# Optimization experiments

Hardware: AMD Instinct MI355X
Metric: run time of the kernel (lower is better)

## Reference

```python
import jax, jax.numpy as jnp
import numpy as np

B, T, D, H = 2, 1024, 1024, 16
HS = D // H
EPS = 1e-5
SCALE = float(np.sqrt(HS))  # faithful bug: scores / hs**(-0.5) == scores * sqrt(hs)


def setup_inputs() -> dict:
    key = jax.random.key(0)
    ks = jax.random.split(key, 20)
    n = lambda k, shape: jax.random.normal(k, shape, dtype=jnp.float32) * 0.02
    return {
        "src": jax.random.normal(ks[0], (B, T, D), dtype=jnp.float32),
        "att": jax.random.normal(ks[1], (B, T, D), dtype=jnp.float32),
        # causal masked self-attention (no biases on q/k/v)
        "wq_m": n(ks[2], (H, D, HS)), "wk_m": n(ks[3], (H, D, HS)), "wv_m": n(ks[4], (H, D, HS)),
        "proj_m_w": n(ks[5], (D, D)), "proj_m_b": jnp.zeros((D,), jnp.float32),
        # final (cross) attention (biases on q/k/v)
        "wq_f": n(ks[6], (H, D, HS)), "wk_f": n(ks[7], (H, D, HS)), "wv_f": n(ks[8], (H, D, HS)),
        "bq_f": jnp.zeros((H, HS), jnp.float32), "bk_f": jnp.zeros((H, HS), jnp.float32),
        "bv_f": jnp.zeros((H, HS), jnp.float32),
        "proj_f_w": n(ks[9], (D, D)), "proj_f_b": jnp.zeros((D,), jnp.float32),
        # FFN
        "w1": n(ks[10], (D, 4 * D)), "b1": jnp.zeros((4 * D,), jnp.float32),
        "w2": n(ks[11], (4 * D, D)), "b2": jnp.zeros((D,), jnp.float32),
        # shared RMSNorm weight (one instance reused at all three sites)
        "norm_w": jnp.ones((D,), jnp.float32),
    }


def rmsnorm(x, w):
    return x * jax.lax.rsqrt(jnp.mean(x * x, axis=-1, keepdims=True) + EPS) * w


def masked_attn(x, wq, wk, wv):
    q = jnp.einsum('btd,hde->bhte', x, wq)
    k = jnp.einsum('btd,hde->bhte', x, wk)
    v = jnp.einsum('btd,hde->bhte', x, wv)
    scores = jnp.einsum('bhte,bhse->bhts', q, k) * SCALE  # [B,H,T,T]
    causal = jnp.tril(jnp.ones((T, T), dtype=bool))
    scores = jnp.where(causal, scores, -jnp.inf)
    a = jax.nn.softmax(scores, axis=-1)
    o = jnp.einsum('bhts,bhse->bhte', a, v)
    return o.transpose(0, 2, 1, 3).reshape(B, T, D)  # concat heads


def final_attn(x, att, wq, bq, wk, bk, wv, bv):
    q = jnp.einsum('btd,hde->bhte', att, wq) + bq[None, :, None, :]
    k = jnp.einsum('btd,hde->bhte', att, wk) + bk[None, :, None, :]
    v = jnp.einsum('btd,hde->bhte', x, wv) + bv[None, :, None, :]
    scores = jnp.einsum('bhte,bhse->bhts', q, k) * SCALE
    a = jax.nn.softmax(scores, axis=-1)
    o = jnp.einsum('bhts,bhse->bhte', a, v)
    return o.transpose(0, 2, 1, 3).reshape(B, T, D)


def reference(src, att, wq_m, wk_m, wv_m, proj_m_w, proj_m_b,
              wq_f, wk_f, wv_f, bq_f, bk_f, bv_f, proj_f_w, proj_f_b,
              w1, b1, w2, b2, norm_w):
    # masked self-attention block
    m = masked_attn(rmsnorm(src, norm_w), wq_m, wk_m, wv_m)
    m_out = src + (m @ proj_m_w + proj_m_b)
    # cross attention block (q/k from norm(att), v from m_out)
    f = final_attn(m_out, rmsnorm(att, norm_w), wq_f, bq_f, wk_f, bk_f, wv_f, bv_f)
    f_out = m_out + (f @ proj_f_w + proj_f_b)
    # FFN block
    h = rmsnorm(f_out, norm_w)
    h = jax.nn.gelu(h @ w1 + b1, approximate=False) @ w2 + b2
    return f_out + h
```

## Files before the change

kernel.cpp:

```cpp
#include <hip/hip_runtime.h>
#include <math.h>

#define BB 2
#define TT 1024
#define DD 1024
#define HH 16
#define HS 64
#define NROWS (BB*TT)

typedef _Float16 f16;
typedef __attribute__((ext_vector_type(8))) _Float16 half8;
typedef __attribute__((ext_vector_type(4))) _Float16 half4;
typedef __attribute__((ext_vector_type(4))) float f32x4;

constexpr float EPS   = 1e-5f;
constexpr float SCALE = 8.0f;

__device__ __forceinline__ void load_lds16(const f16* g, f16* l) {
    __builtin_amdgcn_global_load_lds(
        (const __attribute__((address_space(1))) unsigned int*)g,
        (__attribute__((address_space(3))) unsigned int*)l, 16, 0, 0);
}

__device__ __forceinline__ int xcd_swizzle(int lin, int total) {
    if ((total & 7) == 0) {
        const int chunk = total >> 3;
        lin = (lin & 7) * chunk + (lin >> 3);
    }
    return lin;
}

__global__ __launch_bounds__(256) void prologue_all(
    const float* __restrict__ wq_m, const float* __restrict__ wk_m,
    const float* __restrict__ wv_m, const float* __restrict__ proj_m_w,
    const float* __restrict__ wq_f, const float* __restrict__ wk_f,
    const float* __restrict__ wv_f, const float* __restrict__ proj_f_w,
    const float* __restrict__ w1,   const float* __restrict__ w2,
    f16* __restrict__ wt,
    const float* __restrict__ bq, const float* __restrict__ bk,
    float* __restrict__ biascat,
    const float* __restrict__ src, const float* __restrict__ att,
    const float* __restrict__ normw,
    f16* __restrict__ xn_s, f16* __restrict__ xn_a)
{
    const int bid = blockIdx.x;
    const int tid = threadIdx.x;
    const size_t M_ = 1024 * 1024;

    __shared__ float tt[64][65];

    if (bid == 4096) {
        for (int j = tid; j < 5120; j += 256)
            biascat[j] = (j < 3072) ? 0.f : ((j < 4096) ? bq[j - 3072] : bk[j - 4096]);
        return;
    }

    if (bid > 4096) {
        const int rrow = bid - 4097;
        const int row  = rrow & (NROWS - 1);
        const float* xr = ((rrow < NROWS) ? src : att) + (size_t)row * DD;
        f16* out = ((rrow < NROWS) ? xn_s : xn_a) + (size_t)row * DD;

        float4 xv = reinterpret_cast<const float4*>(xr)[tid];
        float ss = xv.x*xv.x + xv.y*xv.y + xv.z*xv.z + xv.w*xv.w;
        float* red = &tt[0][0];
        red[tid] = ss; __syncthreads();
        for (int s = 128; s > 0; s >>= 1) {
            if (tid < s) red[tid] += red[tid + s];
            __syncthreads();
        }
        const float inv = rsqrtf(red[0] * (1.0f / DD) + EPS);
        float4 wv = reinterpret_cast<const float4*>(normw)[tid];
        half4 o;
        o.x = (f16)(xv.x * inv * wv.x);
        o.y = (f16)(xv.y * inv * wv.y);
        o.z = (f16)(xv.z * inv * wv.z);
        o.w = (f16)(xv.w * inv * wv.w);
        *reinterpret_cast<half4*>(&out[tid * 4]) = o;
        return;
    }

    const float* W; f16* Wt; int K, N, lognk, t; bool headw;
    if (bid < 768)       { const int m = bid >> 8;
                           W = (m == 0) ? wq_m : (m == 1) ? wk_m : wv_m;
                           Wt = wt + (size_t)m * M_;
                           K = 1024; N = 1024; lognk = 4; headw = true;  t = bid & 255; }
    else if (bid < 1024) { W = proj_m_w; Wt = wt + 6 * M_;
                           K = 1024; N = 1024; lognk = 4; headw = false; t = bid - 768; }
    else if (bid < 1792) { const int m = (bid - 1024) >> 8;
                           W = (m == 0) ? wq_f : (m == 1) ? wk_f : wv_f;
                           Wt = wt + (size_t)(3 + m) * M_;
                           K = 1024; N = 1024; lognk = 4; headw = true;  t = (bid - 1024) & 255; }
    else if (bid < 2048) { W = proj_f_w; Wt = wt + 7 * M_;
                           K = 1024; N = 1024; lognk = 4; headw = false; t = bid - 1792; }
    else if (bid < 3072) { W = w1; Wt = wt + 8 * M_;
                           K = 1024; N = 4096; lognk = 4; headw = false; t = bid - 2048; }
    else                 { W = w2; Wt = wt + 12 * M_;
                           K = 4096; N = 1024; lognk = 6; headw = false; t = bid - 3072; }

    const int k0 = (t & ((1 << lognk) - 1)) * 64;
    const int n0 = (t >> lognk) * 64;

    #pragma unroll
    for (int r = 0; r < 4; ++r) {
        const int idx = tid + r * 256;
        const int kl  = idx >> 4;
        const int nl4 = (idx & 15) * 4;
        const float* gp;
        if (headw) {
            gp = W + ((size_t)(n0 >> 6) * K + (k0 + kl)) * 64 + nl4;
        } else {
            gp = W + (size_t)(k0 + kl) * N + n0 + nl4;
        }
        float4 v = *reinterpret_cast<const float4*>(gp);
        tt[kl][nl4 + 0] = v.x; tt[kl][nl4 + 1] = v.y;
        tt[kl][nl4 + 2] = v.z; tt[kl][nl4 + 3] = v.w;
    }
    __syncthreads();
    #pragma unroll
    for (int r = 0; r < 4; ++r) {
        const int idx = tid + r * 256;
        const int nl  = idx >> 4;
        const int kl4 = (idx & 15) * 4;
        half4 o;
        o.x = (f16)tt[kl4 + 0][nl];
        o.y = (f16)tt[kl4 + 1][nl];
        o.z = (f16)tt[kl4 + 2][nl];
        o.w = (f16)tt[kl4 + 3][nl];
        *reinterpret_cast<half4*>(&Wt[(size_t)(n0 + nl) * K + k0 + kl4]) = o;
    }
}

template<int BM, int EPI, bool HEADOUT, bool SPLITA, bool OHALF, bool PARTIAL>
__global__ __launch_bounds__(256, 2) void gemm_mfma(
    const f16* __restrict__ A1,
    const f16* __restrict__ A2,
    const f16* __restrict__ Bt,
    const float* __restrict__ bias,
    float* __restrict__ outF,
    f16* __restrict__ outH,
    int N, int K, int splitN)
{
    constexpr int BK = 32;
    constexpr int MI = 4;
    constexpr int NI = (BM == 128) ? 4 : 2;
    constexpr int WN = (BM == 128) ? 64 : 32;
    constexpr int ASLOT = BM * 4;
    constexpr int AINST = ASLOT / 256;

    __shared__ f16 ldsA[2][ASLOT * 8];
    __shared__ f16 ldsB[2][512 * 8];

    const int tid  = threadIdx.x;
    const int lane = tid & 63;
    const int wid  = tid >> 6;
    const int gy = gridDim.y;
    const int lin = xcd_swizzle(blockIdx.y * gridDim.x + blockIdx.x,
                                gridDim.x * gy);
    const int m0 = (lin % gy) * BM;
    const int n0 = (lin / gy) * 128;
    const int wm = (BM == 128) ? (wid >> 1) : 0;
    const int wn = (BM == 128) ? (wid & 1) : wid;

    const int Klen  = K / gridDim.z;
    const int kbase = blockIdx.z * Klen;

    const f16* Aptr = (SPLITA && n0 >= splitN) ? A2 : A1;

    f32x4 acc[MI][NI];
    #pragma unroll
    for (int i = 0; i < MI; ++i)
        #pragma unroll
        for (int j = 0; j < NI; ++j)
            acc[i][j] = (f32x4){0.f, 0.f, 0.f, 0.f};

    auto stage = [&](int buf, int kt) {
        const int k0 = kbase + kt * BK;
        #pragma unroll
        for (int i = 0; i < AINST; ++i) {
            const int s   = (wid * AINST + i) * 64 + lane;
            const int kh  = s / BM;
            const int row = s % BM;
            load_lds16(Aptr + (size_t)(m0 + row) * K + (k0 + kh * 8),
                       &ldsA[buf][s * 8]);
        }
        #pragma unroll
        for (int i = 0; i < 2; ++i) {
            const int s   = (wid * 2 + i) * 64 + lane;
            const int kh  = s >> 7;
            const int col = s & 127;
            load_lds16(Bt + (size_t)(n0 + col) * K + (k0 + kh * 8),
                       &ldsB[buf][s * 8]);
        }
    };

    const int NT = Klen / BK;
    stage(0, 0);
    __syncthreads();
    int cur = 0;
    const int l15 = lane & 15, l4 = lane >> 4;
    for (int kt = 0; kt < NT; ++kt) {
        if (kt + 1 < NT) stage(cur ^ 1, kt + 1);
        half8 af[MI], bfr[NI];
        #pragma unroll
        for (int mi = 0; mi < MI; ++mi)
            af[mi] = *reinterpret_cast<const half8*>(
                &ldsA[cur][(l4 * BM + wm * 64 + mi * 16 + l15) * 8]);
        #pragma unroll
        for (int ni = 0; ni < NI; ++ni)
            bfr[ni] = *reinterpret_cast<const half8*>(
                &ldsB[cur][(l4 * 128 + wn * WN + ni * 16 + l15) * 8]);
        #pragma unroll
        for (int mi = 0; mi < MI; ++mi)
            #pragma unroll
            for (int ni = 0; ni < NI; ++ni)
                acc[mi][ni] = __builtin_amdgcn_mfma_f32_16x16x32_f16(
                    af[mi], bfr[ni], acc[mi][ni], 0, 0, 0);
        __syncthreads();
        cur ^= 1;
    }

    f16* pout = nullptr;
    if (PARTIAL) {
        const size_t MN = (size_t)gridDim.y * BM * N;
        pout = outH + (size_t)blockIdx.z * MN;
    }

    #pragma unroll
    for (int mi = 0; mi < MI; ++mi) {
        #pragma unroll
        for (int ni = 0; ni < NI; ++ni) {
            #pragma unroll
            for (int r = 0; r < 4; ++r) {
                const int row = m0 + wm * 64 + mi * 16 + l4 * 4 + r;
                const int col = n0 + wn * WN + ni * 16 + l15;
                float v = acc[mi][ni][r];
                if (PARTIAL) {
                    pout[(size_t)row * N + col] = (f16)v;
                    continue;
                }
                if (EPI >= 1) v += bias[col];
                if (EPI == 2) v = 0.5f * v * (1.0f + erff(v * 0.70710678118f));
                size_t oidx;
                if (HEADOUT) {
                    const int mat = col >> 10;
                    const int h = (col >> 6) & 15, e = col & 63;
                    const int b = row >> 10, t = row & (TT - 1);
                    oidx = (size_t)mat * ((size_t)NROWS * DD)
                         + ((size_t)((b * HH + h) * TT + t)) * HS + e;
                } else {
                    oidx = (size_t)row * N + col;
                }
                if (OHALF) outH[oidx] = (f16)v;
                else       outF[oidx] = v;
            }
        }
    }
}

template<int MODE>
__global__ __launch_bounds__(256) void reduce_fuse(const f16* __restrict__ part,
                                                   const float* __restrict__ bias,
                                                   const float* __restrict__ residF,
                                                   const f16* __restrict__ residH,
                                                   float* __restrict__ outF,
                                                   f16* __restrict__ outH,
                                                   const float* __restrict__ normw,
                                                   f16* __restrict__ xnout) {
    const size_t MN  = (size_t)NROWS * 1024;
    const int tid = threadIdx.x;
    const size_t idx = ((size_t)blockIdx.x * 256 + tid) * 4;
    float o[4];
    {
        half4 p0 = *reinterpret_cast<const half4*>(part + idx);
        half4 p1 = *reinterpret_cast<const half4*>(part + MN + idx);
        half4 p2 = *reinterpret_cast<const half4*>(part + 2 * MN + idx);
        half4 p3 = *reinterpret_cast<const half4*>(part + 3 * MN + idx);
        float4 bi = *reinterpret_cast<const float4*>(bias + (idx & 1023));
        o[0] = (float)p0.x + (float)p1.x + (float)p2.x + (float)p3.x + bi.x;
        o[1] = (float)p0.y + (float)p1.y + (float)p2.y + (float)p3.y + bi.y;
        o[2] = (float)p0.z + (float)p1.z + (float)p2.z + (float)p3.z + bi.z;
        o[3] = (float)p0.w + (float)p1.w + (float)p2.w + (float)p3.w + bi.w;
    }
    if (MODE == 0 || MODE == 2) {
        float4 rs = *reinterpret_cast<const float4*>(residF + idx);
        o[0] += rs.x; o[1] += rs.y; o[2] += rs.z; o[3] += rs.w;
    } else {
        half4 rh = *reinterpret_cast<const half4*>(residH + idx);
        o[0] += (float)rh.x; o[1] += (float)rh.y; o[2] += (float)rh.z; o[3] += (float)rh.w;
    }

    if (MODE == 0) {
        half4 h;
        h.x = (f16)o[0]; h.y = (f16)o[1]; h.z = (f16)o[2]; h.w = (f16)o[3];
        *reinterpret_cast<half4*>(outH + idx) = h;
        return;
    }

    float4 ov = {o[0], o[1], o[2], o[3]};
    *reinterpret_cast<float4*>(outF + idx) = ov;

    if (MODE == 1) {
        __shared__ float red[256];
        red[tid] = o[0]*o[0] + o[1]*o[1] + o[2]*o[2] + o[3]*o[3];
        __syncthreads();
        for (int s = 128; s > 0; s >>= 1) {
            if (tid < s) red[tid] += red[tid + s];
            __syncthreads();
        }
        const float inv = rsqrtf(red[0] * (1.0f / DD) + EPS);
        float4 nw = *reinterpret_cast<const float4*>(normw + (idx & 1023));
        half4 h;
        h.x = (f16)(o[0] * inv * nw.x);
        h.y = (f16)(o[1] * inv * nw.y);
        h.z = (f16)(o[2] * inv * nw.z);
        h.w = (f16)(o[3] * inv * nw.w);
        *reinterpret_cast<half4*>(xnout + idx) = h;
    }
}

__global__ __launch_bounds__(256) void reduce_gelu(const f16* __restrict__ part,
                                                   const float* __restrict__ b1,
                                                   f16* __restrict__ h1out) {
    const size_t MN  = (size_t)NROWS * 4096;
    const size_t idx = ((size_t)blockIdx.x * 256 + threadIdx.x) * 4;
    half4 p0 = *reinterpret_cast<const half4*>(part + idx);
    half4 p1 = *reinterpret_cast<const half4*>(part + MN + idx);
    float4 bi = *reinterpret_cast<const float4*>(b1 + (idx & 4095));
    float o[4];
    o[0] = (float)p0.x + (float)p1.x + bi.x;
    o[1] = (float)p0.y + (float)p1.y + bi.y;
    o[2] = (float)p0.z + (float)p1.z + bi.z;
    o[3] = (float)p0.w + (float)p1.w + bi.w;
    half4 h;
    #pragma unroll
    for (int j = 0; j < 4; ++j)
        o[j] = 0.5f * o[j] * (1.0f + erff(o[j] * 0.70710678118f));
    h.x = (f16)o[0]; h.y = (f16)o[1]; h.z = (f16)o[2]; h.w = (f16)o[3];
    *reinterpret_cast<half4*>(h1out + idx) = h;
}

template<bool CAUSAL>
__global__ __launch_bounds__(256) void attn_mfma(const f16* __restrict__ Q,
                                                 const f16* __restrict__ Kg,
                                                 const f16* __restrict__ Vg,
                                                 f16* __restrict__ O) {
    const int iq  = blockIdx.x;
    const int bh  = blockIdx.y;
    const int tid = threadIdx.x;
    const int lane = tid & 63;
    const int w   = tid >> 6;
    const int l15 = lane & 15, l4 = lane >> 4;

    __shared__ f16 Ks[512 * 8];
    __shared__ f16 VT[64 * 72];
    __shared__ f16 Ps[4][16 * 72];

    const f16* qb = Q  + ((size_t)bh * TT + (size_t)iq * 64) * HS;
    const f16* kb = Kg + (size_t)bh * TT * HS;
    const f16* vb = Vg + (size_t)bh * TT * HS;

    half8 qf[2];
    #pragma unroll
    for (int ks = 0; ks < 2; ++ks)
        qf[ks] = *reinterpret_cast<const half8*>(
            qb + (size_t)(w * 16 + l15) * HS + ks * 32 + l4 * 8);

    f32x4 oacc[4];
    #pragma unroll
    for (int ni = 0; ni < 4; ++ni) oacc[ni] = (f32x4){0.f, 0.f, 0.f, 0.f};
    float m_run[4], l_run[4];
    #pragma unroll
    for (int r = 0; r < 4; ++r) { m_run[r] = -1e30f; l_run[r] = 0.f; }

    const int sp  = lane & 31;
    const int ehv = lane >> 5;
    const int c0  = w * 16 + ehv * 8;

    const int ntiles = CAUSAL ? (iq + 1) : (TT / 64);
    for (int js = 0; js < ntiles; ++js) {
        __syncthreads();

        #pragma unroll
        for (int i = 0; i < 2; ++i) {
            const int slot = (w * 2 + i) * 64 + lane;
            load_lds16(kb + (size_t)(js * 64 + (slot & 63)) * HS + (slot >> 6) * 8,
                       &Ks[slot * 8]);
        }
        {
            const f16* vrow = vb + (size_t)(js * 64 + 2 * sp) * HS + c0;
            uint4 r0 = *reinterpret_cast<const uint4*>(vrow);
            uint4 r1 = *reinterpret_cast<const uint4*>(vrow + HS);
            const unsigned rc0[4] = {r0.x, r0.y, r0.z, r0.w};
            const unsigned rc1[4] = {r1.x, r1.y, r1.z, r1.w};
            #pragma unroll
            for (int i = 0; i < 8; ++i) {
                const unsigned lo = (i & 1) ? (rc0[i >> 1] >> 16) : (rc0[i >> 1] & 0xffffu);
                const unsigned hi = (i & 1) ? (rc1[i >> 1] >> 16) : (rc1[i >> 1] & 0xffffu);
                *reinterpret_cast<unsigned*>(&VT[(c0 + i) * 72 + 2 * sp]) = lo | (hi << 16);
            }
        }
        __syncthreads();

        f32x4 sacc[4];
        #pragma unroll
        for (int ni = 0; ni < 4; ++ni) sacc[ni] = (f32x4){0.f, 0.f, 0.f, 0.f};
        __builtin_amdgcn_s_setprio(1);
        #pragma unroll
        for (int ks = 0; ks < 2; ++ks) {
            #pragma unroll
            for (int ni = 0; ni < 4; ++ni) {
                half8 kf = *reinterpret_cast<const half8*>(
                    &Ks[((ks * 4 + l4) * 64 + ni * 16 + l15) * 8]);
                sacc[ni] = __builtin_amdgcn_mfma_f32_16x16x32_f16(qf[ks], kf, sacc[ni], 0, 0, 0);
            }
        }
        __builtin_amdgcn_s_setprio(0);

        float sv[4][4];
        #pragma unroll
        for (int ni = 0; ni < 4; ++ni) {
            #pragma unroll
            for (int r = 0; r < 4; ++r) {
                float x = sacc[ni][r] * SCALE;
                if (CAUSAL && js == iq) {
                    const int sg = js * 64 + ni * 16 + l15;
                    const int qg = iq * 64 + w * 16 + l4 * 4 + r;
                    if (sg > qg) x = -1e30f;
                }
                sv[ni][r] = x;
            }
        }

        #pragma unroll
        for (int r = 0; r < 4; ++r) {
            float rm = fmaxf(fmaxf(sv[0][r], sv[1][r]), fmaxf(sv[2][r], sv[3][r]));
            rm = fmaxf(rm, __shfl_xor(rm, 1));
            rm = fmaxf(rm, __shfl_xor(rm, 2));
            rm = fmaxf(rm, __shfl_xor(rm, 4));
            rm = fmaxf(rm, __shfl_xor(rm, 8));
            const float mnew = fmaxf(m_run[r], rm);
            const float corr = __expf(m_run[r] - mnew);
            float p0 = __expf(sv[0][r] - mnew);
            float p1 = __expf(sv[1][r] - mnew);
            float p2 = __expf(sv[2][r] - mnew);
            float p3 = __expf(sv[3][r] - mnew);
            float sum = p0 + p1 + p2 + p3;
            sum += __shfl_xor(sum, 1);
            sum += __shfl_xor(sum, 2);
            sum += __shfl_xor(sum, 4);
            sum += __shfl_xor(sum, 8);
            l_run[r] = l_run[r] * corr + sum;
            m_run[r] = mnew;
            #pragma unroll
            for (int ni = 0; ni < 4; ++ni) oacc[ni][r] *= corr;
            f16* prow = &Ps[w][(l4 * 4 + r) * 72];
            prow[ 0 + l15] = (f16)p0;
            prow[16 + l15] = (f16)p1;
            prow[32 + l15] = (f16)p2;
            prow[48 + l15] = (f16)p3;
        }

        __builtin_amdgcn_s_setprio(1);
        #pragma unroll
        for (int ks = 0; ks < 2; ++ks) {
            half8 pf = *reinterpret_cast<const half8*>(&Ps[w][l15 * 72 + ks * 32 + l4 * 8]);
            #pragma unroll
            for (int ni = 0; ni < 4; ++ni) {
                half8 vf = *reinterpret_cast<const half8*>(
                    &VT[(ni * 16 + l15) * 72 + ks * 32 + l4 * 8]);
                oacc[ni] = __builtin_amdgcn_mfma_f32_16x16x32_f16(pf, vf, oacc[ni], 0, 0, 0);
            }
        }
        __builtin_amdgcn_s_setprio(0);
    }

    const int b = bh >> 4, h = bh & (HH - 1);
    #pragma unroll
    for (int r = 0; r < 4; ++r) {
        const float inv = 1.0f / l_run[r];
        const int t = iq * 64 + w * 16 + l4 * 4 + r;
        #pragma unroll
        for (int ni = 0; ni < 4; ++ni)
            O[((size_t)(b * TT + t)) * DD + h * HS + ni * 16 + l15] =
                (f16)(oacc[ni][r] * inv);
    }
}

extern "C" void kernel_launch(void* const* d_in, const int* in_sizes, int n_in,
                              void* d_out, int out_size, void* d_ws, size_t ws_size,
                              hipStream_t stream) {
    const float* src      = (const float*)d_in[0];
    const float* att      = (const float*)d_in[1];
    const float* wq_m     = (const float*)d_in[2];
    const float* wk_m     = (const float*)d_in[3];
    const float* wv_m     = (const float*)d_in[4];
    const float* proj_m_w = (const float*)d_in[5];
    const float* proj_m_b = (const float*)d_in[6];
    const float* wq_f     = (const float*)d_in[7];
    const float* wk_f     = (const float*)d_in[8];
    const float* wv_f     = (const float*)d_in[9];
    const float* bq_f     = (const float*)d_in[10];
    const float* bk_f     = (const float*)d_in[11];
    const float* bv_f     = (const float*)d_in[12];
    const float* proj_f_w = (const float*)d_in[13];
    const float* proj_f_b = (const float*)d_in[14];
    const float* w1       = (const float*)d_in[15];
    const float* b1       = (const float*)d_in[16];
    const float* w2       = (const float*)d_in[17];
    const float* b2       = (const float*)d_in[18];
    const float* norm_w   = (const float*)d_in[19];

    const size_t M_ = 1024 * 1024;
    f16* wsb = (f16*)d_ws;
    f16* wt      = wsb;
    f16* headbuf = wsb + 16 * M_;
    f16* h1      = wsb + 16 * M_;
    f16* xn_s    = wsb + 28 * M_;
    f16* xn_a    = wsb + 30 * M_;
    f16* ao      = wsb + 32 * M_;
    f16* mo_h    = wsb + 34 * M_;
    f16* partH   = wsb + 36 * M_;
    f16* partW1  = wsb + 28 * M_;
    f16* xn2     = wsb + 44 * M_;
    float* biascat = (float*)d_out;
    float* f_out = (float*)d_out;
    float* outp  = (float*)d_out;
    (void)ws_size; (void)in_sizes; (void)n_in;

    const dim3 blk(256);
    const int BIG = 1 << 30;
    const dim3 gQKV(40, 16);
    const dim3 gVF(8, 32);
    const dim3 gW1(32, 16, 2);
    const dim3 gSPLIT(8, 16, 4);
    const dim3 gRED(2048);
    const dim3 gREDW1(8192);

    prologue_all<<<dim3(8193), blk, 0, stream>>>(
        wq_m, wk_m, wv_m, proj_m_w, wq_f, wk_f, wv_f, proj_f_w, w1, w2,
        wt, bq_f, bk_f, biascat, src, att, norm_w, xn_s, xn_a);

    gemm_mfma<128, 1, true, true, true, false><<<gQKV, blk, 0, stream>>>(
        xn_s, xn_a, wt, biascat, nullptr, headbuf, 5120, 1024, 3072);

    attn_mfma<true><<<dim3(16, 32), blk, 0, stream>>>(
        headbuf, headbuf + 2 * M_, headbuf + 4 * M_, ao);
    gemm_mfma<128, 0, false, false, false, true><<<gSPLIT, blk, 0, stream>>>(
        ao, nullptr, wt + 6 * M_, nullptr, nullptr, partH, 1024, 1024, BIG);
    reduce_fuse<0><<<gRED, blk, 0, stream>>>(
        partH, proj_m_b, src, nullptr, nullptr, mo_h, nullptr, nullptr);

    gemm_mfma<64, 1, true, false, true, false><<<gVF, blk, 0, stream>>>(
        mo_h, nullptr, wt + 5 * M_, bv_f, nullptr, headbuf + 10 * M_, 1024, 1024, BIG);
    attn_mfma<false><<<dim3(16, 32), blk, 0, stream>>>(
        headbuf + 6 * M_, headbuf + 8 * M_, headbuf + 10 * M_, ao);
    gemm_mfma<128, 0, false, false, false, true><<<gSPLIT, blk, 0, stream>>>(
        ao, nullptr, wt + 7 * M_, nullptr, nullptr, partH, 1024, 1024, BIG);
    reduce_fuse<1><<<gRED, blk, 0, stream>>>(
        partH, proj_f_b, nullptr, mo_h, f_out, nullptr, norm_w, xn2);

    gemm_mfma<128, 0, false, false, false, true><<<gW1, blk, 0, stream>>>(
        xn2, nullptr, wt + 8 * M_, nullptr, nullptr, partW1, 4096, 1024, BIG);
    reduce_gelu<<<gREDW1, blk, 0, stream>>>(partW1, b1, h1);
    gemm_mfma<128, 0, false, false, false, true><<<gSPLIT, blk, 0, stream>>>(
        h1, nullptr, wt + 12 * M_, nullptr, nullptr, partH, 1024, 4096, BIG);
    reduce_fuse<2><<<gRED, blk, 0, stream>>>(
        partH, b2, f_out, nullptr, outp, nullptr, nullptr, nullptr);
}
```

Baseline: 310.4 us.

## Rebalance split-K: split V-proj GEMM, fuse GELU into W1 GEMM, pair causal tiles

```diff
diff --git a/kernel.cpp b/kernel.cpp
--- a/kernel.cpp
+++ b/kernel.cpp
@@ -319,25 +319,26 @@
     }
 }
 
-__global__ __launch_bounds__(256) void reduce_gelu(const f16* __restrict__ part,
-                                                   const float* __restrict__ b1,
-                                                   f16* __restrict__ h1out) {
-    const size_t MN  = (size_t)NROWS * 4096;
-    const size_t idx = ((size_t)blockIdx.x * 256 + threadIdx.x) * 4;
+__global__ __launch_bounds__(256) void reduce_vf(const f16* __restrict__ part,
+                                                 const float* __restrict__ bv,
+                                                 f16* __restrict__ out) {
+    const size_t MN = (size_t)NROWS * 1024;
+    const int t   = blockIdx.x;
+    const int tid = threadIdx.x;
+    const int n   = tid * 4;
+    const size_t idx = (size_t)t * 1024 + n;
     half4 p0 = *reinterpret_cast<const half4*>(part + idx);
     half4 p1 = *reinterpret_cast<const half4*>(part + MN + idx);
-    float4 bi = *reinterpret_cast<const float4*>(b1 + (idx & 4095));
-    float o[4];
-    o[0] = (float)p0.x + (float)p1.x + bi.x;
-    o[1] = (float)p0.y + (float)p1.y + bi.y;
-    o[2] = (float)p0.z + (float)p1.z + bi.z;
-    o[3] = (float)p0.w + (float)p1.w + bi.w;
-    half4 h;
-    #pragma unroll
-    for (int j = 0; j < 4; ++j)
-        o[j] = 0.5f * o[j] * (1.0f + erff(o[j] * 0.70710678118f));
-    h.x = (f16)o[0]; h.y = (f16)o[1]; h.z = (f16)o[2]; h.w = (f16)o[3];
-    *reinterpret_cast<half4*>(h1out + idx) = h;
+    float4 bi = *reinterpret_cast<const float4*>(bv + n);
+    half4 o;
+    o.x = (f16)((float)p0.x + (float)p1.x + bi.x);
+    o.y = (f16)((float)p0.y + (float)p1.y + bi.y);
+    o.z = (f16)((float)p0.z + (float)p1.z + bi.z);
+    o.w = (f16)((float)p0.w + (float)p1.w + bi.w);
+    const int b = t >> 10, tl = t & (TT - 1);
+    const int h = n >> 6, e = n & (HS - 1);
+    *reinterpret_cast<half4*>(
+        &out[((size_t)(b * HH + h) * TT + tl) * HS + e]) = o;
 }
 
 template<bool CAUSAL>
@@ -345,8 +346,13 @@
                                                  const f16* __restrict__ Kg,
                                                  const f16* __restrict__ Vg,
                                                  f16* __restrict__ O) {
-    const int iq  = blockIdx.x;
-    const int bh  = blockIdx.y;
+    int iq, bh;
+    if (CAUSAL) {
+        bh = blockIdx.y;
+        iq = (blockIdx.y < 16) ? blockIdx.x : (15 - blockIdx.x);
+    } else {
+        iq = blockIdx.x; bh = blockIdx.y;
+    }
     const int tid = threadIdx.x;
     const int lane = tid & 63;
     const int w   = tid >> 6;
@@ -521,7 +527,6 @@
     f16* ao      = wsb + 32 * M_;
     f16* mo_h    = wsb + 34 * M_;
     f16* partH   = wsb + 36 * M_;
-    f16* partW1  = wsb + 28 * M_;
     f16* xn2     = wsb + 44 * M_;
     float* biascat = (float*)d_out;
     float* f_out = (float*)d_out;
@@ -531,11 +536,10 @@
     const dim3 blk(256);
     const int BIG = 1 << 30;
     const dim3 gQKV(40, 16);
-    const dim3 gVF(8, 32);
-    const dim3 gW1(32, 16, 2);
+    const dim3 gVF(8, 32, 2);
+    const dim3 gW1(32, 16);
     const dim3 gSPLIT(8, 16, 4);
     const dim3 gRED(2048);
-    const dim3 gREDW1(8192);
 
     prologue_all<<<dim3(8193), blk, 0, stream>>>(
         wq_m, wk_m, wv_m, proj_m_w, wq_f, wk_f, wv_f, proj_f_w, w1, w2,
@@ -551,8 +555,9 @@
     reduce_fuse<0><<<gRED, blk, 0, stream>>>(
         partH, proj_m_b, src, nullptr, nullptr, mo_h, nullptr, nullptr);
 
-    gemm_mfma<64, 1, true, false, true, false><<<gVF, blk, 0, stream>>>(
-        mo_h, nullptr, wt + 5 * M_, bv_f, nullptr, headbuf + 10 * M_, 1024, 1024, BIG);
+    gemm_mfma<64, 0, false, false, false, true><<<gVF, blk, 0, stream>>>(
+        mo_h, nullptr, wt + 5 * M_, nullptr, nullptr, partH, 1024, 1024, BIG);
+    reduce_vf<<<dim3(NROWS), blk, 0, stream>>>(partH, bv_f, headbuf + 10 * M_);
     attn_mfma<false><<<dim3(16, 32), blk, 0, stream>>>(
         headbuf + 6 * M_, headbuf + 8 * M_, headbuf + 10 * M_, ao);
     gemm_mfma<128, 0, false, false, false, true><<<gSPLIT, blk, 0, stream>>>(
@@ -560,9 +565,8 @@
     reduce_fuse<1><<<gRED, blk, 0, stream>>>(
         partH, proj_f_b, nullptr, mo_h, f_out, nullptr, norm_w, xn2);
 
-    gemm_mfma<128, 0, false, false, false, true><<<gW1, blk, 0, stream>>>(
-        xn2, nullptr, wt + 8 * M_, nullptr, nullptr, partW1, 4096, 1024, BIG);
-    reduce_gelu<<<gREDW1, blk, 0, stream>>>(partW1, b1, h1);
+    gemm_mfma<128, 2, false, false, true, false><<<gW1, blk, 0, stream>>>(
+        xn2, nullptr, wt + 8 * M_, b1, nullptr, h1, 4096, 1024, BIG);
     gemm_mfma<128, 0, false, false, false, true><<<gSPLIT, blk, 0, stream>>>(
         h1, nullptr, wt + 12 * M_, nullptr, nullptr, partH, 1024, 4096, BIG);
     reduce_fuse<2><<<gRED, blk, 0, stream>>>(
```

New measurement: 295.7 us. 1.05x faster.
